# Optimization experiments

Hardware: AMD Instinct MI355X
Metric: run time of the kernel (lower is better)

## Reference

```python
import jax, jax.numpy as jnp
import numpy as np

D_MODEL = 1024
N_HEADS = 16
D_HEAD = D_MODEL // N_HEADS


def setup_inputs() -> dict:
    key = jax.random.key(0)
    k1, k2, k3 = jax.random.split(key, 3)
    B, T = 4, 2048
    x = jax.random.normal(k1, (B, T, D_MODEL), dtype=jnp.float32)
    # torch Linear(d, 3d, bias=False): y = x @ W.T ; we store W already transposed -> [d, 3d]
    w_qkv = jax.random.normal(k2, (D_MODEL, 3 * D_MODEL), dtype=jnp.float32) * (D_MODEL ** -0.5)
    w_proj = jax.random.normal(k3, (D_MODEL, D_MODEL), dtype=jnp.float32) * (D_MODEL ** -0.5)
    return {"x": x, "w_qkv": w_qkv, "w_proj": w_proj}


def reference(x, w_qkv, w_proj):
    B, T, C = x.shape
    H, Dh = N_HEADS, D_HEAD
    qkv = (x @ w_qkv).reshape(B, T, 3, H, Dh)
    q = jnp.transpose(qkv[:, :, 0], (0, 2, 1, 3))  # [B,H,T,Dh]
    k = jnp.transpose(qkv[:, :, 1], (0, 2, 1, 3))
    v = jnp.transpose(qkv[:, :, 2], (0, 2, 1, 3))
    scale = 1.0 / jnp.sqrt(jnp.asarray(Dh, dtype=x.dtype))
    att = jnp.einsum('bhqd,bhkd->bhqk', q, k) * scale  # [B,H,T,T]
    causal = jnp.tril(jnp.ones((T, T), dtype=bool))
    att = jnp.where(causal[None, None], att, jnp.asarray(-jnp.inf, dtype=att.dtype))
    att = jax.nn.softmax(att, axis=-1)
    y = jnp.einsum('bhqk,bhkd->bhqd', att, v)          # [B,H,T,Dh]
    y = jnp.transpose(y, (0, 2, 1, 3)).reshape(B, T, C)
    return y @ w_proj
```

## Files before the change

### kernel.cpp

```cpp
#include <hip/hip_runtime.h>
#include <hip/hip_bf16.h>
#include <cmath>

#define T_SEQ 2048
#define NHEADS 16
#define DHEAD 64
#define DMODEL 1024
#define CQKV 3072

typedef __attribute__((ext_vector_type(8))) short short8;
typedef __attribute__((ext_vector_type(8))) __bf16 bf16x8;
typedef __attribute__((ext_vector_type(4))) float floatx4;

#define LDS_CAST(p) ((__attribute__((address_space(3))) void*)(p))
#define GLB_CAST(p) ((const __attribute__((address_space(1))) void*)(p))

static __device__ __forceinline__ floatx4 mfma_bf16(short8 a, short8 b, floatx4 c) {
  return __builtin_amdgcn_mfma_f32_16x16x32_bf16(
      __builtin_bit_cast(bf16x8, a), __builtin_bit_cast(bf16x8, b), c, 0, 0, 0);
}

static __device__ __forceinline__ short f2bf(float f) {
  union { float f; unsigned u; } x; x.f = f;
  unsigned r = x.u + 0x7FFFu + ((x.u >> 16) & 1u);
  return (short)(r >> 16);
}

static __device__ __forceinline__ float bf2f(short s) {
  return __builtin_bit_cast(float, ((unsigned)(unsigned short)s) << 16);
}

static __device__ __forceinline__ float exp2_(float x) {
#if __has_builtin(__builtin_amdgcn_exp2f)
  return __builtin_amdgcn_exp2f(x);
#else
  return exp2f(x);
#endif
}

static __device__ __forceinline__ bool sniff_is_bf16(const unsigned* __restrict__ x) {
  int cnt = 0;
#pragma unroll
  for (int i = 0; i < 32; ++i) {
    unsigned e = (x[i] >> 7) & 0xFFu;
    cnt += (e >= 0x70u && e <= 0x8Fu) ? 1 : 0;
  }
  return cnt >= 16;
}

static __device__ __forceinline__ short8 load8f32(const char* p, size_t idx) {
  const float4* f = (const float4*)(p + idx * 4);
  float4 a = f[0], b = f[1];
  short8 r;
  r[0] = f2bf(a.x); r[1] = f2bf(a.y); r[2] = f2bf(a.z); r[3] = f2bf(a.w);
  r[4] = f2bf(b.x); r[5] = f2bf(b.y); r[6] = f2bf(b.z); r[7] = f2bf(b.w);
  return r;
}

__global__ __launch_bounds__(256) void conv_x(const char* __restrict__ x,
                                              short* __restrict__ o, int n,
                                              const unsigned* __restrict__ xs) {
  const bool isbf = sniff_is_bf16(xs);
  const int i = (blockIdx.x * 256 + threadIdx.x) * 8;
  if (i >= n) return;
  if (isbf) *(short8*)(o + i) = *(const short8*)((const short*)x + i);
  else      *(short8*)(o + i) = load8f32(x, (size_t)i);
}

__global__ __launch_bounds__(256) void tpose(const char* __restrict__ w,
                                             short* __restrict__ wt, int K, int N,
                                             const unsigned* __restrict__ xs) {
  const bool isbf = sniff_is_bf16(xs);
  __shared__ short tile[32][33];
  const int n0 = blockIdx.x * 32, k0 = blockIdx.y * 32;
  const int tx = threadIdx.x & 31, ty = threadIdx.x >> 5;
#pragma unroll
  for (int i = 0; i < 4; ++i) {
    const int r = ty * 4 + i;
    const size_t off = (size_t)(k0 + r) * N + n0 + tx;
    tile[r][tx] = isbf ? ((const short*)w)[off] : f2bf(((const float*)w)[off]);
  }
  __syncthreads();
#pragma unroll
  for (int i = 0; i < 4; ++i) {
    const int r = ty * 4 + i;
    wt[(size_t)(n0 + r) * K + k0 + tx] = tile[tx][r];
  }
}

__global__ __launch_bounds__(256) void gemm128(const short* __restrict__ A,
                                               const short* __restrict__ Bt,
                                               void* __restrict__ C,
                                               short* __restrict__ C2,
                                               int M, int N, int K, int mode,
                                               const unsigned* __restrict__ xs) {
  const bool out_f32 = (mode == 1) ? !sniff_is_bf16(xs) : false;

  __shared__ short as[128 * 32];
  __shared__ short bs[128 * 32];
  const int tid = threadIdx.x;
  const int wid = tid >> 6, lane = tid & 63;
  const int quad = lane >> 4, l16 = lane & 15;
  const int wm = wid >> 1, wn = wid & 1;
  const int m0 = blockIdx.y * 128, n0 = blockIdx.x * 128;

  const int srow = wid * 16 + (lane >> 2);
  const int skc = ((lane & 3) ^ ((lane >> 2) & 3)) * 8;

  const floatx4 zero4 = {0.f, 0.f, 0.f, 0.f};
  floatx4 acc[4][4];
#pragma unroll
  for (int i = 0; i < 4; ++i)
#pragma unroll
    for (int j = 0; j < 4; ++j) acc[i][j] = zero4;

  const int rslot = (quad ^ (l16 & 3)) * 8;

  for (int kt = 0; kt < K; kt += 32) {
    __syncthreads();
#pragma unroll
    for (int r = 0; r < 2; ++r) {
      const short* ga = A + (size_t)(m0 + r * 64 + srow) * K + kt + skc;
      const short* gb = Bt + (size_t)(n0 + r * 64 + srow) * K + kt + skc;
      __builtin_amdgcn_global_load_lds(GLB_CAST(ga), LDS_CAST(as + r * 2048 + wid * 512), 16, 0, 0);
      __builtin_amdgcn_global_load_lds(GLB_CAST(gb), LDS_CAST(bs + r * 2048 + wid * 512), 16, 0, 0);
    }
    __syncthreads();

    short8 afr[4], bfr[4];
#pragma unroll
    for (int mt = 0; mt < 4; ++mt)
      afr[mt] = *(const short8*)&as[(wm * 64 + mt * 16 + l16) * 32 + rslot];
#pragma unroll
    for (int nt = 0; nt < 4; ++nt)
      bfr[nt] = *(const short8*)&bs[(wn * 64 + nt * 16 + l16) * 32 + rslot];
#pragma unroll
    for (int mt = 0; mt < 4; ++mt)
#pragma unroll
      for (int nt = 0; nt < 4; ++nt)
        acc[mt][nt] = mfma_bf16(afr[mt], bfr[nt], acc[mt][nt]);
  }

  const int row0 = m0 + wm * 64 + quad * 4;
  const int col0 = n0 + wn * 64 + l16;
  if (mode == 2 && n0 >= 2048) {
#pragma unroll
    for (int mt = 0; mt < 4; ++mt)
#pragma unroll
      for (int nt = 0; nt < 4; ++nt)
#pragma unroll
        for (int r = 0; r < 4; ++r) {
          const int row = row0 + mt * 16 + r;
          const int col = col0 + nt * 16;
          const int d = col & 63, hh = (col >> 6) - 32;
          const int bb = row >> 11, t = row & 2047;
          C2[((size_t)(bb * 16 + hh) * 64 + d) * T_SEQ + t] = f2bf(acc[mt][nt][r]);
        }
  } else {
    const int outN = (mode == 2) ? 2048 : N;
#pragma unroll
    for (int mt = 0; mt < 4; ++mt)
#pragma unroll
      for (int nt = 0; nt < 4; ++nt)
#pragma unroll
        for (int r = 0; r < 4; ++r) {
          const size_t off = (size_t)(row0 + mt * 16 + r) * outN + col0 + nt * 16;
          if (out_f32) ((float*)C)[off] = acc[mt][nt][r];
          else         ((short*)C)[off] = f2bf(acc[mt][nt][r]);
        }
  }
}

__global__ __launch_bounds__(256) void attn(const short* __restrict__ qk,
                                            const short* __restrict__ vT,
                                            short* __restrict__ y) {
  __shared__ short ks[64 * 64];
  __shared__ short vs[64 * 64];
  __shared__ short ps[4][16][72];
  const int tid = threadIdx.x;
  const int wid = tid >> 6, lane = tid & 63;
  const int quad = lane >> 4, l16 = lane & 15;
  const int b = blockIdx.x >> 4, h = blockIdx.x & 15;
  const int q0 = ((int)gridDim.y - 1 - (int)blockIdx.y) * 64;
  const int qw0 = q0 + wid * 16;

  const short* qbase = qk + (size_t)b * T_SEQ * 2048 + h * DHEAD;
  const short* kbase = qbase + DMODEL;
  const short* vtb = vT + (size_t)(b * NHEADS + h) * DHEAD * T_SEQ;
  const float SC = 0.18033688011112042f;

  short8 aq[2];
#pragma unroll
  for (int kc = 0; kc < 2; ++kc) {
    short8 raw = *(const short8*)(qbase + (size_t)(qw0 + l16) * 2048 + kc * 32 + quad * 8);
#pragma unroll
    for (int j = 0; j < 8; ++j) aq[kc][j] = f2bf(bf2f(raw[j]) * SC);
  }

  const floatx4 zero4 = {0.f, 0.f, 0.f, 0.f};
  floatx4 o[4], lacc = zero4;
#pragma unroll
  for (int i = 0; i < 4; ++i) o[i] = zero4;
  const short8 ones8 = {0x3F80, 0x3F80, 0x3F80, 0x3F80, 0x3F80, 0x3F80, 0x3F80, 0x3F80};

  const int srl = lane >> 3;
  const int sch = ((lane & 7) ^ srl) * 8;

  const int kend = q0 + 64;
  for (int kt = 0; kt < kend; kt += 64) {
    __syncthreads();
#pragma unroll
    for (int i = 0; i < 2; ++i) {
      const int row = i * 32 + wid * 8 + srl;
      const short* gk = kbase + (size_t)(kt + row) * 2048 + sch;
      const short* gv = vtb + (size_t)row * T_SEQ + kt + sch;
      __builtin_amdgcn_global_load_lds(GLB_CAST(gk), LDS_CAST(ks + (i * 32 + wid * 8) * 64), 16, 0, 0);
      __builtin_amdgcn_global_load_lds(GLB_CAST(gv), LDS_CAST(vs + (i * 32 + wid * 8) * 64), 16, 0, 0);
    }
    __syncthreads();

    floatx4 s[4];
#pragma unroll
    for (int nt = 0; nt < 4; ++nt) {
      s[nt] = zero4;
#pragma unroll
      for (int kc = 0; kc < 2; ++kc) {
        const int slot = ((kc * 4 + quad) ^ (l16 & 7)) * 8;
        const short8 bk = *(const short8*)&ks[(nt * 16 + l16) * 64 + slot];
        s[nt] = mfma_bf16(aq[kc], bk, s[nt]);
      }
    }

    const bool full = (kt + 63 <= qw0);
#pragma unroll
    for (int nt = 0; nt < 4; ++nt)
#pragma unroll
      for (int r = 0; r < 4; ++r) {
        float p = exp2_(s[nt][r]);
        if (!full) {
          const int key = kt + nt * 16 + l16;
          const int q = qw0 + quad * 4 + r;
          p = (key <= q) ? p : 0.f;
        }
        s[nt][r] = p;
      }

#pragma unroll
    for (int nt = 0; nt < 4; ++nt)
#pragma unroll
      for (int r = 0; r < 4; ++r)
        ps[wid][quad * 4 + r][nt * 16 + l16] = f2bf(s[nt][r]);

#pragma unroll
    for (int kc = 0; kc < 2; ++kc) {
      const short8 ap = *(const short8*)&ps[wid][l16][kc * 32 + quad * 8];
      lacc = mfma_bf16(ap, ones8, lacc);
#pragma unroll
      for (int d4 = 0; d4 < 4; ++d4) {
        const int slot = ((kc * 4 + quad) ^ (l16 & 7)) * 8;
        const short8 bv = *(const short8*)&vs[(d4 * 16 + l16) * 64 + slot];
        o[d4] = mfma_bf16(ap, bv, o[d4]);
      }
    }
  }

  floatx4 inv;
#pragma unroll
  for (int r = 0; r < 4; ++r) inv[r] = 1.0f / lacc[r];
#pragma unroll
  for (int d4 = 0; d4 < 4; ++d4)
#pragma unroll
    for (int r = 0; r < 4; ++r) {
      const int q = qw0 + quad * 4 + r;
      y[(size_t)(b * T_SEQ + q) * DMODEL + h * DHEAD + d4 * 16 + l16] =
          f2bf(o[d4][r] * inv[r]);
    }
}

extern "C" void kernel_launch(void* const* d_in, const int* in_sizes, int n_in,
                              void* d_out, int out_size, void* d_ws, size_t ws_size,
                              hipStream_t stream) {
  const char* x = (const char*)d_in[0];
  const char* w_qkv = (const char*)d_in[1];
  const char* w_proj = (const char*)d_in[2];
  const unsigned* xs = (const unsigned*)d_in[0];

  short* qk = (short*)d_ws;
  short* vTb = qk + (size_t)8192 * 2048;
  short* wqkvT = vTb + (size_t)64 * 64 * 2048;
  short* wprojT = wqkvT + (size_t)3072 * 1024;
  short* xbf = wprojT + (size_t)1024 * 1024;
  short* ybuf = xbf;

  conv_x<<<8192 * 1024 / (256 * 8), 256, 0, stream>>>(x, xbf, 8192 * 1024, xs);
  {
    dim3 g1(3072 / 32, 1024 / 32);
    tpose<<<g1, 256, 0, stream>>>(w_qkv, wqkvT, 1024, 3072, xs);
    dim3 g2(1024 / 32, 1024 / 32);
    tpose<<<g2, 256, 0, stream>>>(w_proj, wprojT, 1024, 1024, xs);
  }
  {
    dim3 grid(3072 / 128, 8192 / 128);
    gemm128<<<grid, 256, 0, stream>>>(xbf, wqkvT, qk, vTb, 8192, 3072, 1024, 2, xs);
  }
  {
    dim3 grid(4 * NHEADS, T_SEQ / 64);
    attn<<<grid, 256, 0, stream>>>(qk, vTb, ybuf);
  }
  {
    dim3 grid(1024 / 128, 8192 / 128);
    gemm128<<<grid, 256, 0, stream>>>(ybuf, wprojT, d_out, nullptr, 8192, 1024, 1024, 1, xs);
  }
}
```

Baseline: 281.2 us.

## Process two 64-row query tiles per attention block to reuse K/V tiles

Each attention block now handles 128 query rows, with every wave computing two 16-row query tiles against each loaded 64-key K/V tile. K and V fragments are read once from LDS and reused for both tiles, which halves global K/V traffic per query row and the number of blocks launched. The cost is more registers per thread, fewer blocks (reducing parallelism and causal load balance), extra masked work on the diagonal, and an added block-wide barrier per iteration.

```diff
diff --git a/kernel.cpp b/kernel.cpp
--- a/kernel.cpp
+++ b/kernel.cpp
@@ -176,37 +176,41 @@
                                             short* __restrict__ y) {
   __shared__ short ks[64 * 64];
   __shared__ short vs[64 * 64];
-  __shared__ short ps[4][16][72];
+  __shared__ short ps[4][2][16][72];
   const int tid = threadIdx.x;
   const int wid = tid >> 6, lane = tid & 63;
   const int quad = lane >> 4, l16 = lane & 15;
   const int b = blockIdx.x >> 4, h = blockIdx.x & 15;
-  const int q0 = ((int)gridDim.y - 1 - (int)blockIdx.y) * 64;
-  const int qw0 = q0 + wid * 16;
+  const int q0 = ((int)gridDim.y - 1 - (int)blockIdx.y) * 128;
+  const int qw[2] = {q0 + wid * 16, q0 + 64 + wid * 16};
 
   const short* qbase = qk + (size_t)b * T_SEQ * 2048 + h * DHEAD;
   const short* kbase = qbase + DMODEL;
   const short* vtb = vT + (size_t)(b * NHEADS + h) * DHEAD * T_SEQ;
   const float SC = 0.18033688011112042f;
 
-  short8 aq[2];
-#pragma unroll
-  for (int kc = 0; kc < 2; ++kc) {
-    short8 raw = *(const short8*)(qbase + (size_t)(qw0 + l16) * 2048 + kc * 32 + quad * 8);
-#pragma unroll
-    for (int j = 0; j < 8; ++j) aq[kc][j] = f2bf(bf2f(raw[j]) * SC);
-  }
+  short8 aq[2][2];
+#pragma unroll
+  for (int t = 0; t < 2; ++t)
+#pragma unroll
+    for (int kc = 0; kc < 2; ++kc) {
+      short8 raw = *(const short8*)(qbase + (size_t)(qw[t] + l16) * 2048 + kc * 32 + quad * 8);
+#pragma unroll
+      for (int j = 0; j < 8; ++j) aq[t][kc][j] = f2bf(bf2f(raw[j]) * SC);
+    }
 
   const floatx4 zero4 = {0.f, 0.f, 0.f, 0.f};
-  floatx4 o[4], lacc = zero4;
-#pragma unroll
-  for (int i = 0; i < 4; ++i) o[i] = zero4;
+  floatx4 o[2][4], lacc[2] = {zero4, zero4};
+#pragma unroll
+  for (int t = 0; t < 2; ++t)
+#pragma unroll
+    for (int i = 0; i < 4; ++i) o[t][i] = zero4;
   const short8 ones8 = {0x3F80, 0x3F80, 0x3F80, 0x3F80, 0x3F80, 0x3F80, 0x3F80, 0x3F80};
 
   const int srl = lane >> 3;
   const int sch = ((lane & 7) ^ srl) * 8;
 
-  const int kend = q0 + 64;
+  const int kend = q0 + 128;
   for (int kt = 0; kt < kend; kt += 64) {
     __syncthreads();
 #pragma unroll
@@ -219,62 +223,78 @@
     }
     __syncthreads();
 
-    floatx4 s[4];
-#pragma unroll
-    for (int nt = 0; nt < 4; ++nt) {
-      s[nt] = zero4;
-#pragma unroll
-      for (int kc = 0; kc < 2; ++kc) {
+    short8 bk[2][4];
+#pragma unroll
+    for (int kc = 0; kc < 2; ++kc)
+#pragma unroll
+      for (int nt = 0; nt < 4; ++nt) {
         const int slot = ((kc * 4 + quad) ^ (l16 & 7)) * 8;
-        const short8 bk = *(const short8*)&ks[(nt * 16 + l16) * 64 + slot];
-        s[nt] = mfma_bf16(aq[kc], bk, s[nt]);
-      }
-    }
-
-    const bool full = (kt + 63 <= qw0);
-#pragma unroll
-    for (int nt = 0; nt < 4; ++nt)
-#pragma unroll
-      for (int r = 0; r < 4; ++r) {
-        float p = exp2_(s[nt][r]);
-        if (!full) {
-          const int key = kt + nt * 16 + l16;
-          const int q = qw0 + quad * 4 + r;
-          p = (key <= q) ? p : 0.f;
+        bk[kc][nt] = *(const short8*)&ks[(nt * 16 + l16) * 64 + slot];
+      }
+
+#pragma unroll
+    for (int t = 0; t < 2; ++t) {
+      floatx4 s[4];
+#pragma unroll
+      for (int nt = 0; nt < 4; ++nt) {
+        s[nt] = zero4;
+#pragma unroll
+        for (int kc = 0; kc < 2; ++kc) s[nt] = mfma_bf16(aq[t][kc], bk[kc][nt], s[nt]);
+      }
+      const bool full = (kt + 63 <= qw[t]);
+#pragma unroll
+      for (int nt = 0; nt < 4; ++nt)
+#pragma unroll
+        for (int r = 0; r < 4; ++r) {
+          float p = exp2_(s[nt][r]);
+          if (!full) {
+            const int key = kt + nt * 16 + l16;
+            const int q = qw[t] + quad * 4 + r;
+            p = (key <= q) ? p : 0.f;
+          }
+          s[nt][r] = p;
         }
-        s[nt][r] = p;
-      }
-
-#pragma unroll
-    for (int nt = 0; nt < 4; ++nt)
-#pragma unroll
-      for (int r = 0; r < 4; ++r)
-        ps[wid][quad * 4 + r][nt * 16 + l16] = f2bf(s[nt][r]);
+#pragma unroll
+      for (int nt = 0; nt < 4; ++nt)
+#pragma unroll
+        for (int r = 0; r < 4; ++r)
+          ps[wid][t][quad * 4 + r][nt * 16 + l16] = f2bf(s[nt][r]);
+    }
+
+    __syncthreads();
 
 #pragma unroll
     for (int kc = 0; kc < 2; ++kc) {
-      const short8 ap = *(const short8*)&ps[wid][l16][kc * 32 + quad * 8];
-      lacc = mfma_bf16(ap, ones8, lacc);
+      short8 ap[2];
+#pragma unroll
+      for (int t = 0; t < 2; ++t) {
+        ap[t] = *(const short8*)&ps[wid][t][l16][kc * 32 + quad * 8];
+        lacc[t] = mfma_bf16(ap[t], ones8, lacc[t]);
+      }
 #pragma unroll
       for (int d4 = 0; d4 < 4; ++d4) {
         const int slot = ((kc * 4 + quad) ^ (l16 & 7)) * 8;
         const short8 bv = *(const short8*)&vs[(d4 * 16 + l16) * 64 + slot];
-        o[d4] = mfma_bf16(ap, bv, o[d4]);
-      }
-    }
-  }
-
-  floatx4 inv;
-#pragma unroll
-  for (int r = 0; r < 4; ++r) inv[r] = 1.0f / lacc[r];
-#pragma unroll
-  for (int d4 = 0; d4 < 4; ++d4)
-#pragma unroll
-    for (int r = 0; r < 4; ++r) {
-      const int q = qw0 + quad * 4 + r;
-      y[(size_t)(b * T_SEQ + q) * DMODEL + h * DHEAD + d4 * 16 + l16] =
-          f2bf(o[d4][r] * inv[r]);
-    }
+#pragma unroll
+        for (int t = 0; t < 2; ++t) o[t][d4] = mfma_bf16(ap[t], bv, o[t][d4]);
+      }
+    }
+  }
+
+#pragma unroll
+  for (int t = 0; t < 2; ++t) {
+    floatx4 inv;
+#pragma unroll
+    for (int r = 0; r < 4; ++r) inv[r] = 1.0f / lacc[t][r];
+#pragma unroll
+    for (int d4 = 0; d4 < 4; ++d4)
+#pragma unroll
+      for (int r = 0; r < 4; ++r) {
+        const int q = qw[t] + quad * 4 + r;
+        y[(size_t)(b * T_SEQ + q) * DMODEL + h * DHEAD + d4 * 16 + l16] =
+            f2bf(o[t][d4][r] * inv[r]);
+      }
+  }
 }
 
 extern "C" void kernel_launch(void* const* d_in, const int* in_sizes, int n_in,
@@ -304,7 +324,7 @@
     gemm128<<<grid, 256, 0, stream>>>(xbf, wqkvT, qk, vTb, 8192, 3072, 1024, 2, xs);
   }
   {
-    dim3 grid(4 * NHEADS, T_SEQ / 64);
+    dim3 grid(4 * NHEADS, T_SEQ / 128);
     attn<<<grid, 256, 0, stream>>>(qk, vTb, ybuf);
   }
   {
```

Measured after the change: 292.1 us. 3.9% more time.
